# Optimization experiments

Hardware: AMD Instinct MI355X
Metric: run time of the kernel (lower is better)

Reference implementation:

```python
import jax, jax.numpy as jnp
import numpy as np

B, C, H, W = 8, 512, 32, 32


def setup_inputs() -> dict:
    key = jax.random.key(0)
    ks = jax.random.split(key, 7)
    s = 0.02  # typical conv init scale
    return {
        "x": jax.random.normal(ks[0], (B, C, H, W), dtype=jnp.float32),
        "Wq": jax.random.normal(ks[1], (C, C), dtype=jnp.float32) * s,
        "bq": jax.random.normal(ks[2], (C,), dtype=jnp.float32) * s,
        "Wk": jax.random.normal(ks[3], (C, C), dtype=jnp.float32) * s,
        "bk": jax.random.normal(ks[4], (C,), dtype=jnp.float32) * s,
        "W6": jax.random.normal(ks[5], (C, C), dtype=jnp.float32) * s,
        "b6": jax.random.normal(ks[6], (C,), dtype=jnp.float32) * s,
    }


def _gam(x, Wq, bq, Wk, bk, W6, b6):
    b, c, h, w = x.shape
    hw = h * w
    scale = 1.0 / (c ** 0.5)
    # 1x1 convs == per-pixel channel matmuls (torch conv weight [out,in,1,1])
    q = jnp.einsum('bchw,dc->bhwd', x, Wq) + bq          # [B,H,W,C]
    q = q.reshape(b * hw, c)                              # query rows
    k = jnp.einsum('bchw,dc->bdhw', x, Wk) + bk[None, :, None, None]
    k = jnp.transpose(k, (1, 0, 2, 3)).reshape(c, b * hw)  # [C, B*HW]
    xw = (q.astype(jnp.float32) @ k.astype(jnp.float32))   # [B*HW, B*HW]
    xw = xw.reshape(b * hw, b, hw)
    xw = jnp.max(xw, axis=-1)                              # max over keys' spatial dim
    xw = jnp.mean(xw, axis=-1)                             # mean over key images
    xw = xw.reshape(b, hw) * scale
    xw = jax.nn.softmax(xw, axis=-1).astype(x.dtype)
    xw = xw.reshape(b, 1, h, w)
    x5 = x * xw
    return jnp.einsum('bchw,dc->bdhw', x5, W6) + b6[None, :, None, None]


def reference(x, Wq, bq, Wk, bk, W6, b6):
    x_new = _gam(x, Wq, bq, Wk, bk, W6, b6)
    # prototype: mean over batch and spatial dims, keep channels
    x_proto = jnp.mean(x_new.astype(jnp.float32), axis=(0, 2, 3)).astype(x.dtype)
    return x * x_proto[None, :, None, None]
```

## Files before the change

kernel.cpp:

```cpp
#include <hip/hip_runtime.h>
#include <hip/hip_bf16.h>

typedef __bf16 bf16_t;
typedef __bf16 bf16x8 __attribute__((ext_vector_type(8)));
typedef float f32x4 __attribute__((ext_vector_type(4)));

#define B_   8
#define C_   512
#define HW_  1024
#define NPIX 8192

typedef __attribute__((address_space(3))) void lds_vp;
typedef const __attribute__((address_space(1))) void gbl_vp;
__device__ __forceinline__ void gload_lds16(const void* g, void* l) {
    __builtin_amdgcn_global_load_lds((gbl_vp*)g, (lds_vp*)l, 16, 0, 0);
}

__device__ __forceinline__ void stage128x64(const bf16_t* __restrict__ g, int ldk,
                                            bf16_t* lds, int tid) {
    int w64 = tid & ~63;
#pragma unroll
    for (int s = 0; s < 4; ++s) {
        int u = s * 256 + tid;
        const bf16_t* src = g + (size_t)(u >> 3) * ldk + (u & 7) * 8;
        gload_lds16((const void*)src, (void*)(lds + (size_t)(s * 256 + w64) * 8));
    }
}

__global__ void k_cvt_w(const float* __restrict__ Wq, const float* __restrict__ Wk,
                        bf16_t* __restrict__ wq, bf16_t* __restrict__ wk) {
    int i = blockIdx.x * 256 + threadIdx.x;
    wq[i] = (bf16_t)Wq[i];
    wk[i] = (bf16_t)Wk[i];
}

__global__ void k_transpose(const float* __restrict__ x, bf16_t* __restrict__ xT) {
    __shared__ bf16_t tile[64 * 66];
    int p0 = blockIdx.x * 64, c0 = blockIdx.y * 64, b = blockIdx.z;
    int t = threadIdx.x;
#pragma unroll
    for (int s = 0; s < 16; ++s) {
        int u = s * 256 + t;
        int cr = u >> 6, pc = u & 63;
        tile[cr * 66 + pc] = (bf16_t)x[((size_t)(b * C_ + c0 + cr)) * HW_ + p0 + pc];
    }
    __syncthreads();
#pragma unroll
    for (int s = 0; s < 16; ++s) {
        int u = s * 256 + t;
        int pr = u >> 6, cc = u & 63;
        xT[((size_t)(b * HW_ + p0 + pr)) * C_ + c0 + cc] = tile[cc * 66 + pr];
    }
}

__launch_bounds__(256, 2)
__global__ void k_gemm_qk(const bf16_t* __restrict__ xT,
                          const bf16_t* __restrict__ wq, const bf16_t* __restrict__ wk,
                          const float* __restrict__ bq, const float* __restrict__ bk,
                          bf16_t* __restrict__ qo, bf16_t* __restrict__ ko) {
    __shared__ bf16_t As[128 * 64];
    __shared__ bf16_t Bs[128 * 64];
    int bid = blockIdx.x;
    int mtile = bid >> 3;
    int nt = bid & 7;
    const bf16_t* wsel = (nt < 4) ? wq : wk;
    const float*  bsel = (nt < 4) ? bq : bk;
    bf16_t*       osel = (nt < 4) ? qo : ko;
    int nb = (nt & 3) * 128;
    int i0 = mtile * 128;
    int tid = threadIdx.x;
    int lane = tid & 63, w = tid >> 6;
    int wr = w >> 1, wc = w & 1, lr = lane & 15, lg = lane >> 4;

    f32x4 acc[4][4];
#pragma unroll
    for (int mi = 0; mi < 4; ++mi)
#pragma unroll
        for (int ni = 0; ni < 4; ++ni)
#pragma unroll
            for (int r = 0; r < 4; ++r) acc[mi][ni][r] = 0.f;

    for (int kt = 0; kt < 8; ++kt) {
        int k0 = kt * 64;
        stage128x64(xT + (size_t)i0 * 512 + k0, 512, As, tid);
        stage128x64(wsel + (size_t)nb * 512 + k0, 512, Bs, tid);
        __syncthreads();
#pragma unroll
        for (int kk = 0; kk < 2; ++kk) {
            bf16x8 af[4], bfr[4];
#pragma unroll
            for (int mi = 0; mi < 4; ++mi)
                af[mi] = *reinterpret_cast<const bf16x8*>(
                    &As[(wr * 64 + mi * 16 + lr) * 64 + kk * 32 + lg * 8]);
#pragma unroll
            for (int ni = 0; ni < 4; ++ni)
                bfr[ni] = *reinterpret_cast<const bf16x8*>(
                    &Bs[(wc * 64 + ni * 16 + lr) * 64 + kk * 32 + lg * 8]);
#pragma unroll
            for (int mi = 0; mi < 4; ++mi)
#pragma unroll
                for (int ni = 0; ni < 4; ++ni)
                    acc[mi][ni] = __builtin_amdgcn_mfma_f32_16x16x32_bf16(
                        af[mi], bfr[ni], acc[mi][ni], 0, 0, 0);
        }
        __syncthreads();
    }
#pragma unroll
    for (int ni = 0; ni < 4; ++ni) {
        int col = nb + wc * 64 + ni * 16 + lr;
        float bias = bsel[col];
#pragma unroll
        for (int mi = 0; mi < 4; ++mi) {
            int rowb = i0 + wr * 64 + mi * 16 + lg * 4;
#pragma unroll
            for (int r = 0; r < 4; ++r)
                osel[(size_t)(rowb + r) * 512 + col] = (bf16_t)(acc[mi][ni][r] + bias);
        }
    }
}


#define STAGE_A(RH, D, T)                                                          \
    gload_lds16((const void*)(q + srcA + (size_t)((RH) * 128) * 512 +              \
                              ((T) & 7) * 64),                                     \
                (void*)(ldsb + (RH) * 32768 + (D) * 16384 + ldw));                 \
    gload_lds16((const void*)(q + srcA + (size_t)((RH) * 128 + 64) * 512 +         \
                              ((T) & 7) * 64),                                     \
                (void*)(ldsb + (RH) * 32768 + (D) * 16384 + 8192 + ldw));

#define STAGE_B(RH, D, T)                                                          \
    gload_lds16((const void*)(kb + srcB +                                          \
                              (size_t)(((T) >> 3) * 256 + (RH) * 128) * 512 +      \
                              ((T) & 7) * 64),                                     \
                (void*)(ldsb + 65536 + (RH) * 32768 + (D) * 16384 + ldw));         \
    gload_lds16((const void*)(kb + srcB +                                          \
                              (size_t)(((T) >> 3) * 256 + (RH) * 128 + 64) * 512 + \
                              ((T) & 7) * 64),                                     \
                (void*)(ldsb + 65536 + (RH) * 32768 + (D) * 16384 + 8192 + ldw));

#define PHASE(RSET, RD, RKH, RMH, RBF, RBSET, CSET, CMH, CBSET, STG, VM)           \
    {                                                                              \
        const char* rAb = ldsb + wr * 32768 + (RD) * 16384;                        \
        _Pragma("unroll")                                                          \
        for (int mi = 0; mi < 4; ++mi)                                             \
            af[RSET][mi] = *(const bf16x8*)(rAb + (aswz ^ ((RKH) * 64)) +          \
                                            ((RMH) * 4 + mi) * 2048);              \
        if (RBF) {                                                                 \
            const char* rBb = ldsb + 65536 + (wc >> 1) * 32768 + (RD) * 16384;     \
            _Pragma("unroll")                                                      \
            for (int ni = 0; ni < 4; ++ni)                                         \
                bf[RBSET][ni] = *(const bf16x8*)(rBb + (bswz ^ ((RKH) * 64)) +     \
                                                 ni * 2048);                       \
        }                                                                          \
        STG;                                                                       \
        __builtin_amdgcn_s_setprio(1);                                             \
        _Pragma("unroll")                                                          \
        for (int mi = 0; mi < 4; ++mi)                                             \
            _Pragma("unroll")                                                      \
            for (int ni = 0; ni < 4; ++ni)                                         \
                acc[(CMH) * 4 + mi][ni] = __builtin_amdgcn_mfma_f32_16x16x32_bf16( \
                    af[CSET][mi], bf[CBSET][ni], acc[(CMH) * 4 + mi][ni], 0, 0, 0);\
        __builtin_amdgcn_s_setprio(0);                                             \
        VM;                                                                        \
        __builtin_amdgcn_s_barrier();                                              \
    }

__global__ __launch_bounds__(512, 2)
void k_gemm_max8(const bf16_t* __restrict__ q, const bf16_t* __restrict__ kp,
                 float* __restrict__ Mout) {
    __shared__ __align__(16) bf16_t lds[65536];
    char* ldsb = (char*)lds;
    int bid = blockIdx.x;
    int img = bid & 7;
    int qp = bid >> 3;
    int i0 = qp * 256;
    const bf16_t* kb = kp + (size_t)img * HW_ * C_;
    int tid = threadIdx.x;
    int lane = tid & 63, w = tid >> 6;
    int wr = w >> 2, wc = w & 3;
    int lr = lane & 15, lg = lane >> 4;
    int kswz = (lg ^ (lr & 7)) << 4;
    int aswz = lr * 128 + kswz;
    int bswz = ((wc & 1) * 64 + lr) * 128 + kswz;

    int srow = tid >> 3;
    int sk = (((tid & 7) ^ ((tid >> 3) & 7))) << 3;
    size_t srcA = (size_t)(i0 + srow) * 512 + sk;
    size_t srcB = (size_t)srow * 512 + sk;
    int ldw = (tid >> 6) * 1024;

    f32x4 acc[8][4];
    bf16x8 af[2][4], bf[2][4];
    float rm[8][4];
#pragma unroll
    for (int mi = 0; mi < 8; ++mi)
#pragma unroll
        for (int ni = 0; ni < 4; ++ni)
#pragma unroll
            for (int r = 0; r < 4; ++r) acc[mi][ni][r] = 0.f;
#pragma unroll
    for (int mi = 0; mi < 8; ++mi)
#pragma unroll
        for (int r = 0; r < 4; ++r) rm[mi][r] = -3.4e38f;

    STAGE_B(0, 0, 0) STAGE_B(1, 0, 0) STAGE_A(0, 0, 0) STAGE_A(1, 0, 0)
    STAGE_B(0, 1, 1) STAGE_B(1, 1, 1)
    asm volatile("s_waitcnt vmcnt(4)" ::: "memory");
    __builtin_amdgcn_s_barrier();
    {
        const char* rAb = ldsb + wr * 32768;
#pragma unroll
        for (int mi = 0; mi < 4; ++mi)
            af[0][mi] = *(const bf16x8*)(rAb + aswz + mi * 2048);
        const char* rBb = ldsb + 65536 + (wc >> 1) * 32768;
#pragma unroll
        for (int ni = 0; ni < 4; ++ni)
            bf[0][ni] = *(const bf16x8*)(rBb + bswz + ni * 2048);
    }

    for (int i = 0; i < 16; ++i) {
        int tb = 2 * i + 1, tc = 2 * i + 2, td = 2 * i + 3;
        bool s = (i < 15);
        PHASE(1, 0, 0, 1, 0, 0,  0, 0, 0, { STAGE_A(0, 1, tb) }, {})
        PHASE(0, 0, 1, 0, 1, 1,  1, 1, 0, { STAGE_A(1, 1, tb) }, {})
        PHASE(1, 0, 1, 1, 0, 0,  0, 0, 1, {},
              { asm volatile("s_waitcnt vmcnt(0)" ::: "memory"); })
        PHASE(0, 1, 0, 0, 1, 0,  1, 1, 1,
              { if (s) { STAGE_B(0, 0, tc) STAGE_B(1, 0, tc) } }, {})
        PHASE(1, 1, 0, 1, 0, 0,  0, 0, 0, { if (s) { STAGE_A(0, 0, tc) } }, {})
        PHASE(0, 1, 1, 0, 1, 1,  1, 1, 0, { if (s) { STAGE_A(1, 0, tc) } }, {})
        PHASE(1, 1, 1, 1, 0, 0,  0, 0, 1, {},
              { asm volatile("s_waitcnt vmcnt(0)" ::: "memory"); })
        PHASE(0, 0, 0, 0, 1, 0,  1, 1, 1,
              { if (s) { STAGE_B(0, 1, td) STAGE_B(1, 1, td) } }, {})
        if ((i & 3) == 3) {
#pragma unroll
            for (int mi = 0; mi < 8; ++mi)
#pragma unroll
                for (int r = 0; r < 4; ++r) {
                    float v = fmaxf(fmaxf(acc[mi][0][r], acc[mi][1][r]),
                                    fmaxf(acc[mi][2][r], acc[mi][3][r]));
                    rm[mi][r] = fmaxf(rm[mi][r], v);
#pragma unroll
                    for (int ni = 0; ni < 4; ++ni) acc[mi][ni][r] = 0.f;
                }
        }
    }

#pragma unroll
    for (int mi = 0; mi < 8; ++mi)
#pragma unroll
        for (int r = 0; r < 4; ++r) {
            float v = rm[mi][r];
#pragma unroll
            for (int off = 1; off < 16; off <<= 1) v = fmaxf(v, __shfl_xor(v, off));
            rm[mi][r] = v;
        }
    float* sm = (float*)lds;
    if (lr == 0) {
#pragma unroll
        for (int mi = 0; mi < 8; ++mi)
#pragma unroll
            for (int r = 0; r < 4; ++r)
                sm[wc * 256 + wr * 128 + mi * 16 + lg * 4 + r] = rm[mi][r];
    }
    __syncthreads();
    if (tid < 256) {
        float v = fmaxf(fmaxf(sm[tid], sm[256 + tid]),
                        fmaxf(sm[512 + tid], sm[768 + tid]));
        Mout[(size_t)(i0 + tid) * 8 + img] = v;
    }
}

__global__ void k_softmax(const float* __restrict__ Mout, float* __restrict__ wsm) {
    int b = blockIdx.x;
    int t = threadIdx.x;
    __shared__ float red[16];
    const float scale = 0.044194173824159216f;
    float s[4];
#pragma unroll
    for (int i = 0; i < 4; ++i) {
        int p = t + i * 256;
        const float* row = &Mout[(size_t)(b * 1024 + p) * 8];
        float acc = 0.f;
#pragma unroll
        for (int j = 0; j < 8; ++j) acc += row[j];
        s[i] = acc * (scale / 8.0f);
    }
    float m = fmaxf(fmaxf(s[0], s[1]), fmaxf(s[2], s[3]));
#pragma unroll
    for (int off = 1; off < 64; off <<= 1) m = fmaxf(m, __shfl_xor(m, off));
    if ((t & 63) == 0) red[t >> 6] = m;
    __syncthreads();
    float m4 = fmaxf(fmaxf(red[0], red[1]), fmaxf(red[2], red[3]));
    float e[4], sum = 0.f;
#pragma unroll
    for (int i = 0; i < 4; ++i) { e[i] = __expf(s[i] - m4); sum += e[i]; }
#pragma unroll
    for (int off = 1; off < 64; off <<= 1) sum += __shfl_xor(sum, off);
    if ((t & 63) == 0) red[8 + (t >> 6)] = sum;
    __syncthreads();
    float tot = red[8] + red[9] + red[10] + red[11];
    float inv = 1.0f / tot;
#pragma unroll
    for (int i = 0; i < 4; ++i) wsm[b * 1024 + t + i * 256] = e[i] * inv;
}

__global__ void k_reduce_y(const float* __restrict__ x, const float* __restrict__ wsm,
                           float* __restrict__ y) {
    int c = blockIdx.x;
    int t = threadIdx.x;
    float acc = 0.f;
    for (int b = 0; b < 8; ++b) {
        const float* xb = x + ((size_t)(b * C_ + c)) * HW_;
        const float* wb = wsm + b * HW_;
#pragma unroll
        for (int i = 0; i < 4; ++i) {
            int p = t + i * 256;
            acc += xb[p] * wb[p];
        }
    }
#pragma unroll
    for (int off = 1; off < 64; off <<= 1) acc += __shfl_xor(acc, off);
    __shared__ float red[4];
    if ((t & 63) == 0) red[t >> 6] = acc;
    __syncthreads();
    if (t == 0) y[c] = (red[0] + red[1] + red[2] + red[3]) * (1.0f / 8192.0f);
}

__global__ void k_proto(const float* __restrict__ W6, const float* __restrict__ b6,
                        const float* __restrict__ y, float* __restrict__ proto) {
    int d = blockIdx.x;
    int lane = threadIdx.x;
    float acc = 0.f;
#pragma unroll
    for (int i = 0; i < 8; ++i)
        acc += W6[(size_t)d * C_ + lane + i * 64] * y[lane + i * 64];
#pragma unroll
    for (int off = 1; off < 64; off <<= 1) acc += __shfl_xor(acc, off);
    if (lane == 0) proto[d] = acc + b6[d];
}

__global__ void k_final(const float* __restrict__ x, const float* __restrict__ proto,
                        float* __restrict__ out) {
    int idx = blockIdx.x * 256 + threadIdx.x;
    float4 v = ((const float4*)x)[idx];
    int c = (idx >> 8) & 511;
    float p = proto[c];
    v.x *= p; v.y *= p; v.z *= p; v.w *= p;
    ((float4*)out)[idx] = v;
}

extern "C" void kernel_launch(void* const* d_in, const int* in_sizes, int n_in,
                              void* d_out, int out_size, void* d_ws, size_t ws_size,
                              hipStream_t stream) {
    const float* x  = (const float*)d_in[0];
    const float* Wq = (const float*)d_in[1];
    const float* bq = (const float*)d_in[2];
    const float* Wk = (const float*)d_in[3];
    const float* bk = (const float*)d_in[4];
    const float* W6 = (const float*)d_in[5];
    const float* b6 = (const float*)d_in[6];
    float* out = (float*)d_out;

    char* ws = (char*)d_ws;
    bf16_t* xT    = (bf16_t*)(ws);
    float*  Mout  = (float*)(ws);
    bf16_t* wqb   = (bf16_t*)(ws + 8388608);
    bf16_t* wkb   = (bf16_t*)(ws + 8912896);
    bf16_t* qb    = (bf16_t*)(ws + 9437184);
    bf16_t* kb    = (bf16_t*)(ws + 17825792);
    float*  wsm   = (float*)(ws + 26476544);
    float*  yv    = (float*)(ws + 26509312);
    float*  proto = (float*)(ws + 26511360);

    hipLaunchKernelGGL(k_cvt_w, dim3(1024), dim3(256), 0, stream, Wq, Wk, wqb, wkb);
    hipLaunchKernelGGL(k_transpose, dim3(16, 8, 8), dim3(256), 0, stream, x, xT);
    hipLaunchKernelGGL(k_gemm_qk, dim3(512), dim3(256), 0, stream,
                       xT, wqb, wkb, bq, bk, qb, kb);
    hipLaunchKernelGGL(k_gemm_max8, dim3(256), dim3(512), 0, stream, qb, kb, Mout);
    hipLaunchKernelGGL(k_softmax, dim3(8), dim3(256), 0, stream, Mout, wsm);
    hipLaunchKernelGGL(k_reduce_y, dim3(512), dim3(256), 0, stream, x, wsm, yv);
    hipLaunchKernelGGL(k_proto, dim3(512), dim3(64), 0, stream, W6, b6, yv, proto);
    hipLaunchKernelGGL(k_final, dim3(4096), dim3(256), 0, stream, x, proto, out);
}
```

Measured before the change: 103.0 us.

## Swizzle LDS in QK projection GEMM, fuse weight conversion into transpose

Folds the bf16 weight conversion into the transpose kernel, which removes one launch. The QK projection GEMM now stores its staged tiles in LDS with an XOR swizzle so fragment reads avoid bank conflicts. It also replaces __syncthreads with an explicit vmcnt wait plus a raw barrier. A sched_barrier is added before the MFMA block in the max8 GEMM phase macro to keep the compiler from reordering across it. The fused transpose grid is 1024 blocks of 256 threads, which covers exactly the 512x512 weight elements.

```diff
diff --git a/kernel.cpp b/kernel.cpp
--- a/kernel.cpp
+++ b/kernel.cpp
@@ -16,28 +16,28 @@
     __builtin_amdgcn_global_load_lds((gbl_vp*)g, (lds_vp*)l, 16, 0, 0);
 }
 
-__device__ __forceinline__ void stage128x64(const bf16_t* __restrict__ g, int ldk,
-                                            bf16_t* lds, int tid) {
+__device__ __forceinline__ void stage128x64_swz(const bf16_t* __restrict__ g,
+                                                bf16_t* lds, int tid) {
     int w64 = tid & ~63;
 #pragma unroll
     for (int s = 0; s < 4; ++s) {
         int u = s * 256 + tid;
-        const bf16_t* src = g + (size_t)(u >> 3) * ldk + (u & 7) * 8;
+        int row = u >> 3;
+        int kg = (u & 7) ^ (row & 7);
+        const bf16_t* src = g + (size_t)row * 512 + kg * 8;
         gload_lds16((const void*)src, (void*)(lds + (size_t)(s * 256 + w64) * 8));
     }
 }
 
-__global__ void k_cvt_w(const float* __restrict__ Wq, const float* __restrict__ Wk,
-                        bf16_t* __restrict__ wq, bf16_t* __restrict__ wk) {
-    int i = blockIdx.x * 256 + threadIdx.x;
-    wq[i] = (bf16_t)Wq[i];
-    wk[i] = (bf16_t)Wk[i];
-}
-
-__global__ void k_transpose(const float* __restrict__ x, bf16_t* __restrict__ xT) {
+__global__ void k_transpose(const float* __restrict__ x, bf16_t* __restrict__ xT,
+                            const float* __restrict__ Wq, const float* __restrict__ Wk,
+                            bf16_t* __restrict__ wq, bf16_t* __restrict__ wk) {
     __shared__ bf16_t tile[64 * 66];
     int p0 = blockIdx.x * 64, c0 = blockIdx.y * 64, b = blockIdx.z;
     int t = threadIdx.x;
+    int widx = ((blockIdx.z * 8 + blockIdx.y) * 16 + blockIdx.x) * 256 + t;
+    wq[widx] = (bf16_t)Wq[widx];
+    wk[widx] = (bf16_t)Wk[widx];
 #pragma unroll
     for (int s = 0; s < 16; ++s) {
         int u = s * 256 + t;
@@ -58,8 +58,8 @@
                           const bf16_t* __restrict__ wq, const bf16_t* __restrict__ wk,
                           const float* __restrict__ bq, const float* __restrict__ bk,
                           bf16_t* __restrict__ qo, bf16_t* __restrict__ ko) {
-    __shared__ bf16_t As[128 * 64];
-    __shared__ bf16_t Bs[128 * 64];
+    __shared__ __align__(16) bf16_t As[128 * 64];
+    __shared__ __align__(16) bf16_t Bs[128 * 64];
     int bid = blockIdx.x;
     int mtile = bid >> 3;
     int nt = bid & 7;
@@ -71,6 +71,7 @@
     int tid = threadIdx.x;
     int lane = tid & 63, w = tid >> 6;
     int wr = w >> 1, wc = w & 1, lr = lane & 15, lg = lane >> 4;
+    int kswz = (lg ^ (lr & 7)) << 4;
 
     f32x4 acc[4][4];
 #pragma unroll
@@ -82,20 +83,21 @@
 
     for (int kt = 0; kt < 8; ++kt) {
         int k0 = kt * 64;
-        stage128x64(xT + (size_t)i0 * 512 + k0, 512, As, tid);
-        stage128x64(wsel + (size_t)nb * 512 + k0, 512, Bs, tid);
-        __syncthreads();
+        stage128x64_swz(xT + (size_t)i0 * 512 + k0, As, tid);
+        stage128x64_swz(wsel + (size_t)nb * 512 + k0, Bs, tid);
+        asm volatile("s_waitcnt vmcnt(0)" ::: "memory");
+        __builtin_amdgcn_s_barrier();
 #pragma unroll
         for (int kk = 0; kk < 2; ++kk) {
             bf16x8 af[4], bfr[4];
 #pragma unroll
             for (int mi = 0; mi < 4; ++mi)
-                af[mi] = *reinterpret_cast<const bf16x8*>(
-                    &As[(wr * 64 + mi * 16 + lr) * 64 + kk * 32 + lg * 8]);
+                af[mi] = *(const bf16x8*)((const char*)As +
+                    (wr * 64 + mi * 16 + lr) * 128 + (kswz ^ (kk * 64)));
 #pragma unroll
             for (int ni = 0; ni < 4; ++ni)
-                bfr[ni] = *reinterpret_cast<const bf16x8*>(
-                    &Bs[(wc * 64 + ni * 16 + lr) * 64 + kk * 32 + lg * 8]);
+                bfr[ni] = *(const bf16x8*)((const char*)Bs +
+                    (wc * 64 + ni * 16 + lr) * 128 + (kswz ^ (kk * 64)));
 #pragma unroll
             for (int mi = 0; mi < 4; ++mi)
 #pragma unroll
@@ -103,7 +105,7 @@
                     acc[mi][ni] = __builtin_amdgcn_mfma_f32_16x16x32_bf16(
                         af[mi], bfr[ni], acc[mi][ni], 0, 0, 0);
         }
-        __syncthreads();
+        __builtin_amdgcn_s_barrier();
     }
 #pragma unroll
     for (int ni = 0; ni < 4; ++ni) {
@@ -153,6 +155,7 @@
                                                  ni * 2048);                       \
         }                                                                          \
         STG;                                                                       \
+        __builtin_amdgcn_sched_barrier(0);        \
         __builtin_amdgcn_s_setprio(1);                                             \
         _Pragma("unroll")                                                          \
         for (int mi = 0; mi < 4; ++mi)                                             \
@@ -374,8 +377,8 @@
     float*  yv    = (float*)(ws + 26509312);
     float*  proto = (float*)(ws + 26511360);
 
-    hipLaunchKernelGGL(k_cvt_w, dim3(1024), dim3(256), 0, stream, Wq, Wk, wqb, wkb);
-    hipLaunchKernelGGL(k_transpose, dim3(16, 8, 8), dim3(256), 0, stream, x, xT);
+    hipLaunchKernelGGL(k_transpose, dim3(16, 8, 8), dim3(256), 0, stream,
+                       x, xT, Wq, Wk, wqb, wkb);
     hipLaunchKernelGGL(k_gemm_qk, dim3(512), dim3(256), 0, stream,
                        xT, wqb, wkb, bq, bk, qb, kb);
     hipLaunchKernelGGL(k_gemm_max8, dim3(256), dim3(512), 0, stream, qb, kb, Mout);
```

New measurement: 96.09 us. 6.7% less time.
